# Kernel tuning notes

Measured on AMD Instinct MI355X. Metric: run time of the kernel, lower is better.

The kernel has to match this reference:

```python
import jax, jax.numpy as jnp
import numpy as np

N_NODES = 50000
N_EDGES = 500000
V_IN, V_OUT, E_IN, E_OUT = 128, 128, 64, 64
SQRT_TWO = 1.4142135623730951

def _xavier_normal(key, shape, gain):
    fan_in, fan_out = shape
    std = gain * np.sqrt(2.0 / (fan_in + fan_out))
    return jax.random.normal(key, shape, dtype=jnp.float32) * std

def setup_inputs() -> dict:
    key = jax.random.key(0)
    ks = jax.random.split(key, 8)
    cat_dim = 2 * V_IN + E_IN
    return {
        "x": jax.random.normal(ks[0], (N_NODES, V_IN), dtype=jnp.float32),
        "edge_index": jax.random.randint(ks[1], (2, N_EDGES), 0, N_NODES, dtype=jnp.int64),
        "edge_attr": jax.random.normal(ks[2], (N_EDGES, E_IN), dtype=jnp.float32),
        "W_a": _xavier_normal(ks[3], (cat_dim, V_OUT), SQRT_TWO),
        "W_T": _xavier_normal(ks[4], (cat_dim, V_OUT), SQRT_TWO),
        "b_T": jnp.zeros((V_OUT,), dtype=jnp.float32),
        "W_e": _xavier_normal(ks[5], (V_IN, E_OUT), SQRT_TWO),
        "W_ee": _xavier_normal(ks[6], (E_IN, E_OUT), SQRT_TWO),
        "a_prelu": jnp.array(0.25, dtype=jnp.float32),  # PReLU default: single shared slope
    }

def _prelu(x, a):
    return jnp.where(x >= 0, x, a * x)

def _scatter_softmax(src, index, num_segments):
    # src: [E, D], index: [E] -> softmax over edges grouped by index, per column
    seg_max = jax.ops.segment_max(src, index, num_segments=num_segments)  # [N, D]
    ex = jnp.exp(src - seg_max[index])
    seg_sum = jax.ops.segment_sum(ex, index, num_segments=num_segments)  # [N, D]
    return ex / (seg_sum[index] + 1e-16)

def reference(x, edge_index, edge_attr, W_a, W_T, b_T, W_e, W_ee, a_prelu):
    src, dst = edge_index[0], edge_index[1]
    N1 = x[src]          # [E, V_IN]
    N2 = x[dst]          # [E, V_IN]
    e = edge_attr        # [E, E_IN]
    new_e_feat = N1 @ W_e + N2 @ W_e + e @ W_ee          # [E, E_OUT]
    cat = jnp.concatenate([N2, e, N1], axis=1)            # [E, 2V+E]
    attention_logits = _prelu(cat @ W_a, a_prelu)         # [E, V_OUT]
    messages = cat @ W_T                                  # [E, V_OUT]
    attention = _scatter_softmax(attention_logits, dst, x.shape[0])
    agg_msg = attention * messages
    new_x = jax.ops.segment_sum(agg_msg, dst, num_segments=x.shape[0]) + b_T
    return (new_x, new_e_feat)
```

## Files before the change

### kernel.cpp

```cpp
#include <hip/hip_runtime.h>
#include <hip/hip_bf16.h>


typedef float  f32x4   __attribute__((ext_vector_type(4)));
typedef __bf16 bf16x8  __attribute__((ext_vector_type(8)));
typedef unsigned short ushort8_t __attribute__((ext_vector_type(8)));

#define ROWSTRIDE 328

__device__ __forceinline__ unsigned short f2bf(float f) {
  unsigned int u = __float_as_uint(f);
  return (unsigned short)((u + 0x7FFFu + ((u >> 16) & 1u)) >> 16);
}

__device__ __forceinline__ void store_bf4(unsigned short* p, float4 v) {
  ushort4 u;
  u.x = f2bf(v.x); u.y = f2bf(v.y); u.z = f2bf(v.z); u.w = f2bf(v.w);
  *(ushort4*)p = u;
}

__global__ void prep_b_kernel(const float* __restrict__ Wa,
                              const float* __restrict__ Wt,
                              const float* __restrict__ We,
                              const float* __restrict__ Wee,
                              unsigned short* __restrict__ Bp) {
  int pe = blockIdx.x * 256 + threadIdx.x;
  int j    = pe & 7;
  int lane = (pe >> 3) & 63;
  int kt   = (pe >> 9) % 10;
  int nt   = pe / 5120;
  int k = kt * 32 + ((lane >> 4) << 3) + j;
  int n = nt * 16 + (lane & 15);
  float v;
  if (n < 128) {
    v = Wa[k * 128 + n];
  } else if (n < 256) {
    v = Wt[k * 128 + (n - 128)];
  } else {
    int c = n - 256;
    if (k < 128)      v = We[k * 64 + c];
    else if (k < 192) v = Wee[(k - 128) * 64 + c];
    else              v = We[(k - 192) * 64 + c];
  }
  Bp[pe] = f2bf(v);
}

__global__ __launch_bounds__(256, 2) void fused_edge_kernel(
    const float* __restrict__ x,
    const int*   __restrict__ ei,
    const float* __restrict__ ea,
    const unsigned short* __restrict__ Bp,
    float* __restrict__ num,
    float* __restrict__ den,
    float* __restrict__ out_e,
    const float* __restrict__ a_prelu,
    int E) {
  __shared__ unsigned short At[64 * ROWSTRIDE];
  __shared__ int s_src[64];
  __shared__ int s_dst[64];

  const int tid = threadIdx.x;
  const int eb  = blockIdx.x * 64;

  if (tid < 64) {
    int e = eb + tid;
    int s = 0, d = 0;
    if (e < E) { s = ei[e]; d = ei[E + e]; }
    s_src[tid] = s;
    s_dst[tid] = d;
  }
  __syncthreads();

  const float4* x4  = (const float4*)x;
  const float4* ea4 = (const float4*)ea;

  #pragma unroll
  for (int i = tid; i < 2048; i += 256) {
    int r = i >> 5, c4 = i & 31;
    float4 v = {0.f, 0.f, 0.f, 0.f};
    if (eb + r < E) v = x4[(size_t)s_dst[r] * 32 + c4];
    store_bf4(&At[r * ROWSTRIDE + c4 * 4], v);
  }
  #pragma unroll
  for (int i = tid; i < 1024; i += 256) {
    int r = i >> 4, c4 = i & 15;
    float4 v = {0.f, 0.f, 0.f, 0.f};
    if (eb + r < E) v = ea4[(size_t)(eb + r) * 16 + c4];
    store_bf4(&At[r * ROWSTRIDE + 128 + c4 * 4], v);
  }
  #pragma unroll
  for (int i = tid; i < 2048; i += 256) {
    int r = i >> 5, c4 = i & 31;
    float4 v = {0.f, 0.f, 0.f, 0.f};
    if (eb + r < E) v = x4[(size_t)s_src[r] * 32 + c4];
    store_bf4(&At[r * ROWSTRIDE + 192 + c4 * 4], v);
  }
  __syncthreads();

  const int w    = tid >> 6;
  const int l    = tid & 63;
  const int lrow = l & 15;
  const int lk8  = (l >> 4) << 3;

  f32x4 acc[4][5];
  #pragma unroll
  for (int mt = 0; mt < 4; ++mt)
    #pragma unroll
    for (int i = 0; i < 5; ++i)
      acc[mt][i] = (f32x4){0.f, 0.f, 0.f, 0.f};

  for (int kc = 0; kc < 10; ++kc) {
    const int kbase = kc * 32 + lk8;
    bf16x8 av[4];
    #pragma unroll
    for (int mt = 0; mt < 4; ++mt) {
      ushort8_t u = *(const ushort8_t*)&At[(mt * 16 + lrow) * ROWSTRIDE + kbase];
      av[mt] = __builtin_bit_cast(bf16x8, u);
    }
    #pragma unroll
    for (int i = 0; i < 5; ++i) {
      const int nt = w + 4 * i;
      ushort8_t ub = *(const ushort8_t*)&Bp[(((nt * 10 + kc) * 64) + l) * 8];
      bf16x8 bv = __builtin_bit_cast(bf16x8, ub);
      #pragma unroll
      for (int mt = 0; mt < 4; ++mt)
        acc[mt][i] = __builtin_amdgcn_mfma_f32_16x16x32_bf16(av[mt], bv, acc[mt][i], 0, 0, 0);
    }
  }

  const float slope = a_prelu[0];
  const int rbase = (l >> 4) << 2;
  const int ccol  = l & 15;

  #pragma unroll
  for (int mt = 0; mt < 4; ++mt) {
    const int m0 = mt * 16 + rbase;
    #pragma unroll
    for (int r = 0; r < 4; ++r) {
      int m = m0 + r;
      if (eb + m < E)
        out_e[(size_t)(eb + m) * 64 + w * 16 + ccol] = acc[mt][4][r];
    }
    #pragma unroll
    for (int i2 = 0; i2 < 2; ++i2) {
      const int c = (w + 4 * i2) * 16 + ccol;
      #pragma unroll
      for (int r = 0; r < 4; ++r) {
        int m = m0 + r;
        if (eb + m < E) {
          float lg = acc[mt][i2][r];
          float ex = __expf(lg >= 0.f ? lg : slope * lg);
          float mg = acc[mt][i2 + 2][r];
          int d = s_dst[m];
          unsafeAtomicAdd(&num[(size_t)d * 128 + c], ex * mg);
          unsafeAtomicAdd(&den[(size_t)d * 128 + c], ex);
        }
      }
    }
  }
}

__global__ void finalize_kernel(const float* __restrict__ num,
                                const float* __restrict__ den,
                                const float* __restrict__ bT,
                                float* __restrict__ out_x,
                                int total) {
  int i = blockIdx.x * 256 + threadIdx.x;
  if (i < total)
    out_x[i] = num[i] / (den[i] + 1e-16f) + bT[i & 127];
}

extern "C" void kernel_launch(void* const* d_in, const int* in_sizes, int n_in,
                              void* d_out, int out_size, void* d_ws, size_t ws_size,
                              hipStream_t stream) {
  const float* x   = (const float*)d_in[0];
  const int*   ei  = (const int*)d_in[1];
  const float* ea  = (const float*)d_in[2];
  const float* Wa  = (const float*)d_in[3];
  const float* Wt  = (const float*)d_in[4];
  const float* bT  = (const float*)d_in[5];
  const float* We  = (const float*)d_in[6];
  const float* Wee = (const float*)d_in[7];
  const float* ap  = (const float*)d_in[8];

  const int N = in_sizes[0] / 128;
  const int E = in_sizes[1] / 2;

  unsigned short* Bp = (unsigned short*)d_ws;
  float* num = (float*)((char*)d_ws + 204800);
  float* den = num + (size_t)N * 128;

  float* out_x = (float*)d_out;
  float* out_e = out_x + (size_t)N * 128;

  hipMemsetAsync(num, 0, (size_t)N * 128 * 2 * sizeof(float), stream);
  prep_b_kernel<<<400, 256, 0, stream>>>(Wa, Wt, We, Wee, Bp);
  fused_edge_kernel<<<(E + 63) / 64, 256, 0, stream>>>(x, ei, ea, Bp, num, den,
                                                       out_e, ap, E);
  finalize_kernel<<<((size_t)N * 128 + 255) / 256, 256, 0, stream>>>(
      num, den, bT, out_x, N * 128);
}
```

Baseline: 713.9 us.

## Sort edges by destination and pre-reduce segment sums in LDS before atomics

Adds a counting sort of edges by destination (histogram, single-block scan, scatter into a permutation), and the fused edge kernel now processes edges in that sorted order. Within each block, the softmax numerator and denominator contributions are staged in shared memory and summed over runs of equal destination, so each run issues one atomic instead of one per edge. Edge attributes and edge outputs are now gathered and scattered through the permutation, which costs some coalescing. The sort adds three extra launches, including a serial single-block scan, and with about 10 edges per node the runs are short, so fewer atomics may not cover the added cost.

Result: faster. 692.7 us (-3.0%).

```diff
diff --git a/kernel.cpp b/kernel.cpp
--- a/kernel.cpp
+++ b/kernel.cpp
@@ -7,6 +7,7 @@
 typedef unsigned short ushort8_t __attribute__((ext_vector_type(8)));
 
 #define ROWSTRIDE 328
+#define RED_STRIDE 132
 
 __device__ __forceinline__ unsigned short f2bf(float f) {
   unsigned int u = __float_as_uint(f);
@@ -45,27 +46,81 @@
   Bp[pe] = f2bf(v);
 }
 
+__global__ void hist_kernel(const int* __restrict__ ei, int* __restrict__ cnt,
+                            int E) {
+  int e = blockIdx.x * 256 + threadIdx.x;
+  if (e < E) atomicAdd(&cnt[ei[E + e]], 1);
+}
+
+__global__ void scan_kernel(const int* __restrict__ cnt, int* __restrict__ cur,
+                            int n) {
+  __shared__ int ls[1024];
+  const int t = threadIdx.x;
+  const int base = t * 49;
+  int s = 0;
+  for (int i = 0; i < 49; ++i) {
+    int idx = base + i;
+    if (idx < n) s += cnt[idx];
+  }
+  ls[t] = s;
+  __syncthreads();
+  for (int off = 1; off < 1024; off <<= 1) {
+    int v = (t >= off) ? ls[t - off] : 0;
+    __syncthreads();
+    ls[t] += v;
+    __syncthreads();
+  }
+  int run = (t == 0) ? 0 : ls[t - 1];
+  for (int i = 0; i < 49; ++i) {
+    int idx = base + i;
+    if (idx < n) {
+      int v = cnt[idx];
+      cur[idx] = run;
+      run += v;
+    }
+  }
+}
+
+__global__ void scatter_kernel(const int* __restrict__ ei, int* __restrict__ cur,
+                               int* __restrict__ perm, int E) {
+  int e = blockIdx.x * 256 + threadIdx.x;
+  if (e < E) {
+    int d = ei[E + e];
+    int pos = atomicAdd(&cur[d], 1);
+    perm[pos] = e;
+  }
+}
+
 __global__ __launch_bounds__(256, 2) void fused_edge_kernel(
     const float* __restrict__ x,
     const int*   __restrict__ ei,
     const float* __restrict__ ea,
+    const int*   __restrict__ perm,
     const unsigned short* __restrict__ Bp,
     float* __restrict__ num,
     float* __restrict__ den,
     float* __restrict__ out_e,
     const float* __restrict__ a_prelu,
     int E) {
-  __shared__ unsigned short At[64 * ROWSTRIDE];
+  __shared__ __align__(16) char smem[64 * ROWSTRIDE * 2];
+  unsigned short* At = (unsigned short*)smem;
+  float* red = (float*)smem;
   __shared__ int s_src[64];
   __shared__ int s_dst[64];
+  __shared__ int s_eid[64];
 
   const int tid = threadIdx.x;
   const int eb  = blockIdx.x * 64;
+  const int nvalid = min(64, E - eb);
 
   if (tid < 64) {
-    int e = eb + tid;
-    int s = 0, d = 0;
-    if (e < E) { s = ei[e]; d = ei[E + e]; }
+    int e = 0, s = 0, d = 0;
+    if (tid < nvalid) {
+      e = perm[eb + tid];
+      s = ei[e];
+      d = ei[E + e];
+    }
+    s_eid[tid] = e;
     s_src[tid] = s;
     s_dst[tid] = d;
   }
@@ -78,21 +133,21 @@
   for (int i = tid; i < 2048; i += 256) {
     int r = i >> 5, c4 = i & 31;
     float4 v = {0.f, 0.f, 0.f, 0.f};
-    if (eb + r < E) v = x4[(size_t)s_dst[r] * 32 + c4];
+    if (r < nvalid) v = x4[(size_t)s_dst[r] * 32 + c4];
     store_bf4(&At[r * ROWSTRIDE + c4 * 4], v);
   }
   #pragma unroll
   for (int i = tid; i < 1024; i += 256) {
     int r = i >> 4, c4 = i & 15;
     float4 v = {0.f, 0.f, 0.f, 0.f};
-    if (eb + r < E) v = ea4[(size_t)(eb + r) * 16 + c4];
+    if (r < nvalid) v = ea4[(size_t)s_eid[r] * 16 + c4];
     store_bf4(&At[r * ROWSTRIDE + 128 + c4 * 4], v);
   }
   #pragma unroll
   for (int i = tid; i < 2048; i += 256) {
     int r = i >> 5, c4 = i & 31;
     float4 v = {0.f, 0.f, 0.f, 0.f};
-    if (eb + r < E) v = x4[(size_t)s_src[r] * 32 + c4];
+    if (r < nvalid) v = x4[(size_t)s_src[r] * 32 + c4];
     store_bf4(&At[r * ROWSTRIDE + 192 + c4 * 4], v);
   }
   __syncthreads();
@@ -138,23 +193,73 @@
     #pragma unroll
     for (int r = 0; r < 4; ++r) {
       int m = m0 + r;
-      if (eb + m < E)
-        out_e[(size_t)(eb + m) * 64 + w * 16 + ccol] = acc[mt][4][r];
-    }
+      if (m < nvalid)
+        out_e[(size_t)s_eid[m] * 64 + w * 16 + ccol] = acc[mt][4][r];
+    }
+  }
+
+  float exv[4][2][4];
+  #pragma unroll
+  for (int mt = 0; mt < 4; ++mt)
+    #pragma unroll
+    for (int i2 = 0; i2 < 2; ++i2)
+      #pragma unroll
+      for (int r = 0; r < 4; ++r) {
+        float lg = acc[mt][i2][r];
+        exv[mt][i2][r] = __expf(lg >= 0.f ? lg : slope * lg);
+      }
+
+  __syncthreads();
+
+  #pragma unroll
+  for (int mt = 0; mt < 4; ++mt) {
+    const int m0 = mt * 16 + rbase;
     #pragma unroll
     for (int i2 = 0; i2 < 2; ++i2) {
       const int c = (w + 4 * i2) * 16 + ccol;
       #pragma unroll
-      for (int r = 0; r < 4; ++r) {
-        int m = m0 + r;
-        if (eb + m < E) {
-          float lg = acc[mt][i2][r];
-          float ex = __expf(lg >= 0.f ? lg : slope * lg);
-          float mg = acc[mt][i2 + 2][r];
-          int d = s_dst[m];
-          unsafeAtomicAdd(&num[(size_t)d * 128 + c], ex * mg);
-          unsafeAtomicAdd(&den[(size_t)d * 128 + c], ex);
-        }
+      for (int r = 0; r < 4; ++r)
+        red[(m0 + r) * RED_STRIDE + c] = exv[mt][i2][r] * acc[mt][i2 + 2][r];
+    }
+  }
+  __syncthreads();
+  {
+    const int c  = tid & 127;
+    const int r0 = (tid >> 7) * 32;
+    const int r1 = min(r0 + 32, nvalid);
+    float sum = 0.f;
+    for (int r = r0; r < r1; ++r) {
+      sum += red[r * RED_STRIDE + c];
+      if (r == r1 - 1 || s_dst[r + 1] != s_dst[r]) {
+        unsafeAtomicAdd(&num[(size_t)s_dst[r] * 128 + c], sum);
+        sum = 0.f;
+      }
+    }
+  }
+  __syncthreads();
+
+  #pragma unroll
+  for (int mt = 0; mt < 4; ++mt) {
+    const int m0 = mt * 16 + rbase;
+    #pragma unroll
+    for (int i2 = 0; i2 < 2; ++i2) {
+      const int c = (w + 4 * i2) * 16 + ccol;
+      #pragma unroll
+      for (int r = 0; r < 4; ++r)
+        red[(m0 + r) * RED_STRIDE + c] = exv[mt][i2][r];
+    }
+  }
+  __syncthreads();
+  {
+    const int c  = tid & 127;
+    const int r0 = (tid >> 7) * 32;
+    const int r1 = min(r0 + 32, nvalid);
+    float sum = 0.f;
+    for (int r = r0; r < r1; ++r) {
+      sum += red[r * RED_STRIDE + c];
+      if (r == r1 - 1 || s_dst[r + 1] != s_dst[r]) {
+        unsafeAtomicAdd(&den[(size_t)s_dst[r] * 128 + c], sum);
+        sum = 0.f;
       }
     }
   }
@@ -186,17 +291,24 @@
   const int N = in_sizes[0] / 128;
   const int E = in_sizes[1] / 2;
 
-  unsigned short* Bp = (unsigned short*)d_ws;
-  float* num = (float*)((char*)d_ws + 204800);
+  char* ws = (char*)d_ws;
+  unsigned short* Bp = (unsigned short*)ws;
+  float* num = (float*)(ws + 204800);
   float* den = num + (size_t)N * 128;
+  int* cnt   = (int*)(ws + 204800 + (size_t)N * 128 * 8);
+  int* cur   = cnt + 50176;
+  int* perm  = cur + 50176;
 
   float* out_x = (float*)d_out;
   float* out_e = out_x + (size_t)N * 128;
 
-  hipMemsetAsync(num, 0, (size_t)N * 128 * 2 * sizeof(float), stream);
+  hipMemsetAsync(num, 0, (size_t)N * 128 * 8 + 50176 * sizeof(int), stream);
   prep_b_kernel<<<400, 256, 0, stream>>>(Wa, Wt, We, Wee, Bp);
-  fused_edge_kernel<<<(E + 63) / 64, 256, 0, stream>>>(x, ei, ea, Bp, num, den,
-                                                       out_e, ap, E);
+  hist_kernel<<<(E + 255) / 256, 256, 0, stream>>>(ei, cnt, E);
+  scan_kernel<<<1, 1024, 0, stream>>>(cnt, cur, N);
+  scatter_kernel<<<(E + 255) / 256, 256, 0, stream>>>(ei, cur, perm, E);
+  fused_edge_kernel<<<(E + 63) / 64, 256, 0, stream>>>(x, ei, ea, perm, Bp,
+                                                       num, den, out_e, ap, E);
   finalize_kernel<<<((size_t)N * 128 + 255) / 256, 256, 0, stream>>>(
       num, den, bT, out_x, N * 128);
 }
```
